# Optimization experiments

Hardware: AMD Instinct MI355X
Metric: run time of the kernel (lower is better)

## Reference

```python
import jax, jax.numpy as jnp
import numpy as np

# --- Config (Kimi/DeepSeek-style fine-grained MoE) ---
T = 4096        # num tokens
H = 1024        # hidden_size
I = 512         # moe_intermediate_size
E = 64          # num_experts
K = 8           # num_experts_per_token (top_k)
NG = 8          # num_expert_group
TKG = 4         # topk_group
NSH = 2         # num_shared_experts
IS = I * NSH    # shared-expert intermediate size
ROUTED_SCALE = 2.5


def setup_inputs() -> dict:
    key = jax.random.key(0)
    ks = jax.random.split(key, 7)
    s = 0.02
    return {
        "hidden_states": jax.random.normal(ks[0], (T, H), jnp.float32),
        "gate_w": jax.random.normal(ks[1], (E, H), jnp.float32) * s,          # router
        "e_bias": jax.random.normal(ks[2], (E,), jnp.float32) * 0.01,          # e_score_correction_bias
        "w1": jax.random.normal(ks[3], (E, H, 2 * I), jnp.float32) * s,       # per-expert gate_up
        "w2": jax.random.normal(ks[4], (E, I, H), jnp.float32) * s,           # per-expert down
        "sw_gu": jax.random.normal(ks[5], (H, 2 * IS), jnp.float32) * s,      # shared gate_up
        "sw_d": jax.random.normal(ks[6], (IS, H), jnp.float32) * s,           # shared down
    }


def _silu_and_mul(gu):
    d = gu.shape[-1] // 2
    return jax.nn.silu(gu[..., :d]) * gu[..., d:]


def _grouped_topk(scores, e_bias):
    """DeepSeek-V3/Kimi grouped top-k with sigmoid scoring + score-correction bias."""
    Tn = scores.shape[0]
    sfc = scores + e_bias[None, :]                       # scores_for_choice [T, E]
    # group score = sum of top-2 corrected scores inside each group
    grp = sfc.reshape(Tn, NG, E // NG)
    group_scores = jax.lax.top_k(grp, 2)[0].sum(-1)      # [T, NG]
    gidx = jax.lax.top_k(group_scores, TKG)[1]           # [T, TKG]
    gmask = jnp.zeros((Tn, NG), sfc.dtype).at[jnp.arange(Tn)[:, None], gidx].set(1.0)
    smask = jnp.repeat(gmask, E // NG, axis=1) > 0       # [T, E] bool
    tmp = jnp.where(smask, sfc, 0.0)                     # masked_fill(~mask, 0.0) as in vLLM
    topk_ids = jax.lax.top_k(tmp, K)[1]                  # [T, K]
    topk_w = jnp.take_along_axis(scores, topk_ids, axis=1)
    topk_w = topk_w / topk_w.sum(-1, keepdims=True)      # renormalize
    return topk_w, topk_ids


def _forward(x, gate_w, e_bias, w1, w2, sw_gu, sw_d):
    Tn, Hn = x.shape
    # shared experts (KimiMLP)
    shared = _silu_and_mul(x @ sw_gu) @ sw_d             # [T, H]
    # router
    logits = x @ gate_w.T                                # [T, E]
    scores = jax.nn.sigmoid(logits)
    topk_w, topk_ids = _grouped_topk(scores, e_bias)
    # dispatch: sort the T*K assignments by expert id -> grouped GEMM
    flat_ids = topk_ids.reshape(-1)                      # [T*K]
    order = jnp.argsort(flat_ids)                        # [T*K]
    tok = order // K                                     # token index of each sorted assignment
    xs = x[tok]                                          # [T*K, H] gathered tokens
    gsizes = jnp.bincount(flat_ids, length=E).astype(jnp.int32)
    gu = jax.lax.ragged_dot(xs, w1, gsizes)              # [T*K, 2I] grouped GEMM
    h = _silu_and_mul(gu)                                # [T*K, I]
    ys = jax.lax.ragged_dot(h, w2, gsizes)               # [T*K, H]
    # combine: scale by routing weight, scatter-add back to tokens
    flat_w = topk_w.reshape(-1)[order]                   # [T*K]
    routed = jnp.zeros((Tn, Hn), x.dtype).at[tok].add(ys * flat_w[:, None])
    return routed * ROUTED_SCALE + shared


def reference(hidden_states, gate_w, e_bias, w1, w2, sw_gu, sw_d):
    return _forward(hidden_states, gate_w, e_bias, w1, w2, sw_gu, sw_d)
```

## Files before the change

### kernel.cpp

```cpp
#include <hip/hip_runtime.h>
#include <cstdint>
#include <cstddef>

#define TT   4096
#define HH   1024
#define II   512
#define EE   64
#define KT   8
#define ISZ  1024
#define TKA  32768
#define MAXT 320

typedef __bf16 bf16x8 __attribute__((ext_vector_type(8)));
typedef float  f32x4  __attribute__((ext_vector_type(4)));

__device__ __forceinline__ unsigned short f2bf(float f) {
  unsigned u = __float_as_uint(f);
  u += 0x7fffu + ((u >> 16) & 1u);
  return (unsigned short)(u >> 16);
}

#define GLDS(gp, lp) __builtin_amdgcn_global_load_lds( \
    (const __attribute__((address_space(1))) void*)(gp), \
    (__attribute__((address_space(3))) void*)(lp), 16, 0, 0)

__global__ __launch_bounds__(256) void k_transpose(const float* __restrict__ in,
                                                   unsigned short* __restrict__ out,
                                                   int R, int C) {
  __shared__ float tile[64][65];
  long b = blockIdx.z;
  int r0 = blockIdx.x * 64, c0 = blockIdx.y * 64;
  const float* ip = in + b * (long)R * C;
  unsigned short* op = out + b * (long)R * C;
  int tc = threadIdx.x & 63, tr = threadIdx.x >> 6;
#pragma unroll
  for (int rr = 0; rr < 64; rr += 4)
    tile[tr + rr][tc] = ip[(long)(r0 + tr + rr) * C + (c0 + tc)];
  __syncthreads();
#pragma unroll
  for (int rr = 0; rr < 64; rr += 4)
    op[(long)(c0 + tr + rr) * R + (r0 + tc)] = f2bf(tile[tc][tr + rr]);
}

__global__ __launch_bounds__(256) void k_cvt(const float* __restrict__ in,
                                             unsigned short* __restrict__ out) {
  int i = blockIdx.x * 256 + threadIdx.x;
  float4 v = ((const float4*)in)[i];
  ushort4 o;
  o.x = f2bf(v.x); o.y = f2bf(v.y); o.z = f2bf(v.z); o.w = f2bf(v.w);
  ((ushort4*)out)[i] = o;
}

__global__ __launch_bounds__(256) void k_router(const float* __restrict__ x,
    const float* __restrict__ gw, const float* __restrict__ eb,
    int* __restrict__ topk_ids, float* __restrict__ topk_w, int* __restrict__ counts)
{
  __shared__ float xrow[HH];
  __shared__ float sc[EE];
  int t = blockIdx.x;
  int tid = threadIdx.x;
  for (int i = tid; i < HH; i += 256) xrow[i] = x[(long)t * HH + i];
  __syncthreads();
  int e = tid >> 2, q = tid & 3;
  const float* w = gw + (long)e * HH;
  double acc = 0.0, acc2 = 0.0;
  for (int i = q * 8; i < HH; i += 32) {
    float4 wa = *(const float4*)(w + i);
    float4 wb = *(const float4*)(w + i + 4);
    acc  += (double)wa.x * (double)xrow[i]
          + (double)wa.y * (double)xrow[i + 1]
          + (double)wa.z * (double)xrow[i + 2]
          + (double)wa.w * (double)xrow[i + 3];
    acc2 += (double)wb.x * (double)xrow[i + 4]
          + (double)wb.y * (double)xrow[i + 5]
          + (double)wb.z * (double)xrow[i + 6]
          + (double)wb.w * (double)xrow[i + 7];
  }
  acc += acc2;
  acc += __shfl_down(acc, 2);
  acc += __shfl_down(acc, 1);
  if (q == 0) sc[e] = (float)(1.0 / (1.0 + exp(-acc)));
  __syncthreads();
  if (tid < 64) {
    int lane = tid;
    float s = sc[lane];
    float sfc = s + eb[lane];
    float m1 = sfc, m2 = -1e30f;
#pragma unroll
    for (int d = 1; d < 8; d <<= 1) {
      float o1 = __shfl_xor(m1, d);
      float o2 = __shfl_xor(m2, d);
      float hi = fmaxf(m1, o1);
      float lo = fminf(m1, o1);
      m2 = fmaxf(lo, fmaxf(m2, o2));
      m1 = hi;
    }
    float gs = m1 + m2;
    int g = lane >> 3;
    int grank = 0;
#pragma unroll
    for (int j = 0; j < 8; j++) {
      float gj = __shfl(gs, j * 8);
      if (gj > gs || (gj == gs && j < g)) grank++;
    }
    bool gsel = grank < 4;
    float mv = gsel ? sfc : 0.0f;
    int rank = 0;
    for (int j = 0; j < 64; j++) {
      float vj = __shfl(mv, j);
      if (vj > mv || (vj == mv && j < lane)) rank++;
    }
    bool sel = rank < KT;
    float ssum = sel ? s : 0.0f;
#pragma unroll
    for (int d = 1; d < 64; d <<= 1) ssum += __shfl_xor(ssum, d);
    unsigned long long bal = __ballot(sel);
    if (sel) {
      int pos = __popcll(bal & ((1ull << lane) - 1ull));
      topk_ids[(long)t * KT + pos] = lane;
      topk_w[(long)t * KT + pos] = s / ssum;
      atomicAdd(&counts[lane], 1);
    }
  }
}

__global__ void k_offsets(const int* __restrict__ counts, int* __restrict__ offsets,
                          int* __restrict__ cursor, int* __restrict__ tile_e,
                          int* __restrict__ tile_r0)
{
  int lane = threadIdx.x;
  int c = counts[lane];
  int xs = c;
#pragma unroll
  for (int d = 1; d < 64; d <<= 1) { int y = __shfl_up(xs, d); if (lane >= d) xs += y; }
  int off = xs - c;
  offsets[lane] = off;
  cursor[lane] = off;
  if (lane == 63) offsets[EE] = xs;
  int nt = (c + 127) >> 7;
  int tp = nt;
#pragma unroll
  for (int d = 1; d < 64; d <<= 1) { int y = __shfl_up(tp, d); if (lane >= d) tp += y; }
  int tbase = tp - nt;
  for (int i = 0; i < nt; i++) { tile_e[tbase + i] = lane; tile_r0[tbase + i] = off + i * 128; }
  int total = __shfl(tp, 63);
  for (int i = total + lane; i < MAXT; i += 64) tile_e[i] = -1;
}

__global__ __launch_bounds__(256) void k_scatter(const int* __restrict__ ids,
    const float* __restrict__ tw, int* __restrict__ cursor,
    int* __restrict__ perm, float* __restrict__ wslot)
{
  int a = blockIdx.x * 256 + threadIdx.x;
  int e = ids[a];
  int pos = atomicAdd(&cursor[e], 1);
  perm[pos] = a >> 3;
  wslot[pos] = tw[a];
}

__global__ __launch_bounds__(256) void k_gemm_gu(
    const unsigned short* __restrict__ Abase, const int* __restrict__ perm,
    const unsigned short* __restrict__ Bbase, long eStride, int Kd, int upOff,
    unsigned short* __restrict__ Hout,
    const int* __restrict__ tile_e, const int* __restrict__ tile_r0,
    const int* __restrict__ eoff, int rowsTotal)
{
  __shared__ __align__(16) unsigned short lds[8192];
  int e = 0, row0, end;
  if (tile_e) {
    e = tile_e[blockIdx.x];
    if (e < 0) return;
    row0 = tile_r0[blockIdx.x];
    end = eoff[e + 1];
  } else { row0 = blockIdx.x * 128; end = rowsTotal; }
  const unsigned short* B = Bbase + (long)e * eStride;
  int n0 = blockIdx.y * 64;
  int tid = threadIdx.x, lane = tid & 63, wave = tid >> 6;
  int wm = wave >> 1, wn = wave & 1;
  int lr = lane >> 2, lk = (lane & 3) * 8;
  int r0a = row0 + wave * 32 + lr;
  int r1a = r0a + 16;
  int t0 = r0a < rowsTotal ? r0a : rowsTotal - 1;
  int t1 = r1a < rowsTotal ? r1a : rowsTotal - 1;
  if (perm) { t0 = perm[t0]; t1 = perm[t1]; }
  const unsigned short* ap0 = Abase + (long)t0 * Kd + lk;
  const unsigned short* ap1 = Abase + (long)t1 * Kd + lk;
  const unsigned short* bg = B + (long)(n0 + wave * 16 + lr) * Kd + lk;
  const unsigned short* bu = B + (long)(upOff + n0 + wave * 16 + lr) * Kd + lk;
  unsigned short* lA0 = lds + wave * 1024 + lane * 8;
  unsigned short* lBg = lds + 4096 + wave * 512 + lane * 8;
  unsigned short* lBu = lds + 6144 + wave * 512 + lane * 8;
  f32x4 acc[4][4];
  f32x4 z = {0.f, 0.f, 0.f, 0.f};
  for (int i = 0; i < 4; i++) for (int j = 0; j < 4; j++) acc[i][j] = z;
  int quad = lane >> 4, cl = lane & 15;
  for (int k0 = 0; k0 < Kd; k0 += 32) {
    __syncthreads();
    GLDS(ap0 + k0, lA0);
    GLDS(ap1 + k0, lA0 + 512);
    GLDS(bg + k0, lBg);
    GLDS(bu + k0, lBu);
    __syncthreads();
    bf16x8 af[4], bgf[2], buf2[2];
#pragma unroll
    for (int mi = 0; mi < 4; mi++)
      af[mi] = *(const bf16x8*)(lds + (wm * 64 + mi * 16 + cl) * 32 + quad * 8);
#pragma unroll
    for (int ni = 0; ni < 2; ni++) {
      bgf[ni]  = *(const bf16x8*)(lds + 4096 + (wn * 32 + ni * 16 + cl) * 32 + quad * 8);
      buf2[ni] = *(const bf16x8*)(lds + 6144 + (wn * 32 + ni * 16 + cl) * 32 + quad * 8);
    }
#pragma unroll
    for (int mi = 0; mi < 4; mi++) {
#pragma unroll
      for (int ni = 0; ni < 2; ni++) {
        acc[mi][ni]     = __builtin_amdgcn_mfma_f32_16x16x32_bf16(af[mi], bgf[ni],  acc[mi][ni],     0, 0, 0);
        acc[mi][ni + 2] = __builtin_amdgcn_mfma_f32_16x16x32_bf16(af[mi], buf2[ni], acc[mi][ni + 2], 0, 0, 0);
      }
    }
  }
#pragma unroll
  for (int mi = 0; mi < 4; mi++) {
#pragma unroll
    for (int j = 0; j < 2; j++) {
#pragma unroll
      for (int r = 0; r < 4; r++) {
        int row = row0 + wm * 64 + mi * 16 + quad * 4 + r;
        if (row < end) {
          float g = acc[mi][j][r], u = acc[mi][j + 2][r];
          float hv = g * (1.f / (1.f + __expf(-g))) * u;
          Hout[(long)row * upOff + (n0 + wn * 32 + j * 16 + cl)] = f2bf(hv);
        }
      }
    }
  }
}

__global__ __launch_bounds__(256) void k_gemm_down(
    const unsigned short* __restrict__ Abase,
    const unsigned short* __restrict__ Bbase, long eStride, int Kd,
    float* __restrict__ Out,
    const int* __restrict__ perm, const float* __restrict__ wslot,
    const int* __restrict__ tile_e, const int* __restrict__ tile_r0,
    const int* __restrict__ eoff, int rowsTotal, int doAtomic)
{
  __shared__ __align__(16) unsigned short lds[8192];
  int e = 0, row0, end;
  if (tile_e) {
    e = tile_e[blockIdx.x];
    if (e < 0) return;
    row0 = tile_r0[blockIdx.x];
    end = eoff[e + 1];
  } else { row0 = blockIdx.x * 128; end = rowsTotal; }
  const unsigned short* B = Bbase + (long)e * eStride;
  int n0 = blockIdx.y * 128;
  int tid = threadIdx.x, lane = tid & 63, wave = tid >> 6;
  int wm = wave >> 1, wn = wave & 1;
  int lr = lane >> 2, lk = (lane & 3) * 8;
  int r0a = row0 + wave * 32 + lr;
  int r1a = r0a + 16;
  int t0 = r0a < rowsTotal ? r0a : rowsTotal - 1;
  int t1 = r1a < rowsTotal ? r1a : rowsTotal - 1;
  const unsigned short* ap0 = Abase + (long)t0 * Kd + lk;
  const unsigned short* ap1 = Abase + (long)t1 * Kd + lk;
  const unsigned short* bp0 = B + (long)(n0 + wave * 32 + lr) * Kd + lk;
  const unsigned short* bp1 = bp0 + (long)16 * Kd;
  unsigned short* lA0 = lds + wave * 1024 + lane * 8;
  unsigned short* lB0 = lds + 4096 + wave * 1024 + lane * 8;
  f32x4 acc[4][4];
  f32x4 z = {0.f, 0.f, 0.f, 0.f};
  for (int i = 0; i < 4; i++) for (int j = 0; j < 4; j++) acc[i][j] = z;
  int quad = lane >> 4, cl = lane & 15;
  for (int k0 = 0; k0 < Kd; k0 += 32) {
    __syncthreads();
    GLDS(ap0 + k0, lA0);
    GLDS(ap1 + k0, lA0 + 512);
    GLDS(bp0 + k0, lB0);
    GLDS(bp1 + k0, lB0 + 512);
    __syncthreads();
    bf16x8 af[4], bfr[4];
#pragma unroll
    for (int mi = 0; mi < 4; mi++)
      af[mi] = *(const bf16x8*)(lds + (wm * 64 + mi * 16 + cl) * 32 + quad * 8);
#pragma unroll
    for (int ni = 0; ni < 4; ni++)
      bfr[ni] = *(const bf16x8*)(lds + 4096 + (wn * 64 + ni * 16 + cl) * 32 + quad * 8);
#pragma unroll
    for (int mi = 0; mi < 4; mi++)
#pragma unroll
      for (int ni = 0; ni < 4; ni++)
        acc[mi][ni] = __builtin_amdgcn_mfma_f32_16x16x32_bf16(af[mi], bfr[ni], acc[mi][ni], 0, 0, 0);
  }
#pragma unroll
  for (int mi = 0; mi < 4; mi++) {
    int rowb = row0 + wm * 64 + mi * 16 + quad * 4;
#pragma unroll
    for (int r = 0; r < 4; r++) {
      int row = rowb + r;
      if (row >= end) continue;
      long orow = row;
      float scale = 1.f;
      if (doAtomic) { orow = perm[row]; scale = wslot[row] * 2.5f; }
#pragma unroll
      for (int ni = 0; ni < 4; ni++) {
        int col = n0 + wn * 64 + ni * 16 + cl;
        float v = acc[mi][ni][r] * scale;
        if (doAtomic) unsafeAtomicAdd(&Out[orow * HH + col], v);
        else          Out[orow * HH + col] = v;
      }
    }
  }
}

extern "C" void kernel_launch(void* const* d_in, const int* in_sizes, int n_in,
                              void* d_out, int out_size, void* d_ws, size_t ws_size,
                              hipStream_t stream)
{
  const float* x   = (const float*)d_in[0];
  const float* gw  = (const float*)d_in[1];
  const float* eb  = (const float*)d_in[2];
  const float* w1  = (const float*)d_in[3];
  const float* w2  = (const float*)d_in[4];
  const float* sgu = (const float*)d_in[5];
  const float* sd  = (const float*)d_in[6];
  float* out = (float*)d_out;
  char* ws = (char*)d_ws;
  size_t off = 0;
  auto alloc = [&](size_t b) { void* p = ws + off; off += (b + 255) & ~(size_t)255; return p; };
  unsigned short* w1t  = (unsigned short*)alloc((size_t)EE * 2 * II * HH * 2);
  unsigned short* w2t  = (unsigned short*)alloc((size_t)EE * HH * II * 2);
  unsigned short* sgut = (unsigned short*)alloc((size_t)2 * ISZ * HH * 2);
  unsigned short* sdt  = (unsigned short*)alloc((size_t)HH * ISZ * 2);
  unsigned short* xb   = (unsigned short*)alloc((size_t)TT * HH * 2);
  unsigned short* hsb  = (unsigned short*)alloc((size_t)TT * ISZ * 2);
  unsigned short* hb   = (unsigned short*)alloc((size_t)TKA * II * 2);
  int*   tids   = (int*)alloc((size_t)TKA * 4);
  float* tw     = (float*)alloc((size_t)TKA * 4);
  int*   counts = (int*)alloc(256);
  int*   offs   = (int*)alloc(512);
  int*   cursor = (int*)alloc(256);
  int*   tile_e = (int*)alloc(MAXT * 4);
  int*   tile_r = (int*)alloc(MAXT * 4);
  int*   perm   = (int*)alloc((size_t)TKA * 4);
  float* wslot  = (float*)alloc((size_t)TKA * 4);

  hipMemsetAsync(counts, 0, 256, stream);
  dim3 b256(256);
  k_transpose<<<dim3(HH / 64, (2 * II) / 64, EE), b256, 0, stream>>>(w1, w1t, HH, 2 * II);
  k_transpose<<<dim3(II / 64, HH / 64, EE), b256, 0, stream>>>(w2, w2t, II, HH);
  k_transpose<<<dim3(HH / 64, (2 * ISZ) / 64, 1), b256, 0, stream>>>(sgu, sgut, HH, 2 * ISZ);
  k_transpose<<<dim3(ISZ / 64, HH / 64, 1), b256, 0, stream>>>(sd, sdt, ISZ, HH);
  k_cvt<<<dim3((TT * HH) / 1024), b256, 0, stream>>>(x, xb);
  k_router<<<dim3(TT), b256, 0, stream>>>(x, gw, eb, tids, tw, counts);
  k_offsets<<<dim3(1), dim3(64), 0, stream>>>(counts, offs, cursor, tile_e, tile_r);
  k_scatter<<<dim3(TKA / 256), b256, 0, stream>>>(tids, tw, cursor, perm, wslot);
  k_gemm_gu<<<dim3(MAXT, II / 64), b256, 0, stream>>>(xb, perm, w1t, (long)2 * II * HH, HH, II,
                                                      hb, tile_e, tile_r, offs, TKA);
  k_gemm_gu<<<dim3(TT / 128, ISZ / 64), b256, 0, stream>>>(xb, nullptr, sgut, 0, HH, ISZ,
                                                           hsb, nullptr, nullptr, nullptr, TT);
  k_gemm_down<<<dim3(TT / 128, HH / 128), b256, 0, stream>>>(hsb, sdt, 0, ISZ, out,
                                                             nullptr, nullptr, nullptr, nullptr,
                                                             nullptr, TT, 0);
  k_gemm_down<<<dim3(MAXT, HH / 128), b256, 0, stream>>>(hb, w2t, (long)HH * II, II, out,
                                                         perm, wslot, tile_e, tile_r, offs, TKA, 1);
}
```

Before: 1.003 ms.

## Replace atomic scatter-add with bf16 staging plus gather combine; swizzle LDS

The routed down-projection now writes weighted bf16 outputs per sorted slot into a staging buffer instead of doing float atomics into the output. A new combine kernel uses an inverse permutation to gather each token's K expert rows and add them to the shared-expert result. Separately, both GEMMs permute the k-chunk placement when filling LDS and read back with a matching swizzle to reduce bank conflicts. This removes atomic contention at the cost of an extra 64MB bf16 round trip and a bf16 rounding of the routed contributions before summation.

```diff
diff --git a/kernel.cpp b/kernel.cpp
--- a/kernel.cpp
+++ b/kernel.cpp
@@ -13,6 +13,7 @@
 
 typedef __bf16 bf16x8 __attribute__((ext_vector_type(8)));
 typedef float  f32x4  __attribute__((ext_vector_type(4)));
+typedef unsigned short us8v __attribute__((ext_vector_type(8)));
 
 __device__ __forceinline__ unsigned short f2bf(float f) {
   unsigned u = __float_as_uint(f);
@@ -23,6 +24,7 @@
 #define GLDS(gp, lp) __builtin_amdgcn_global_load_lds( \
     (const __attribute__((address_space(1))) void*)(gp), \
     (__attribute__((address_space(3))) void*)(lp), 16, 0, 0)
+
 
 __global__ __launch_bounds__(256) void k_transpose(const float* __restrict__ in,
                                                    unsigned short* __restrict__ out,
@@ -149,13 +151,14 @@
 
 __global__ __launch_bounds__(256) void k_scatter(const int* __restrict__ ids,
     const float* __restrict__ tw, int* __restrict__ cursor,
-    int* __restrict__ perm, float* __restrict__ wslot)
+    int* __restrict__ perm, float* __restrict__ wslot, int* __restrict__ inv)
 {
   int a = blockIdx.x * 256 + threadIdx.x;
   int e = ids[a];
   int pos = atomicAdd(&cursor[e], 1);
   perm[pos] = a >> 3;
   wslot[pos] = tw[a];
+  inv[a] = pos;
 }
 
 __global__ __launch_bounds__(256) void k_gemm_gu(
@@ -177,16 +180,17 @@
   int n0 = blockIdx.y * 64;
   int tid = threadIdx.x, lane = tid & 63, wave = tid >> 6;
   int wm = wave >> 1, wn = wave & 1;
-  int lr = lane >> 2, lk = (lane & 3) * 8;
+  int lr = lane >> 2;
+  int lkq = ((((lane & 3) - ((lane >> 3) & 3)) & 3)) * 8;
   int r0a = row0 + wave * 32 + lr;
   int r1a = r0a + 16;
   int t0 = r0a < rowsTotal ? r0a : rowsTotal - 1;
   int t1 = r1a < rowsTotal ? r1a : rowsTotal - 1;
   if (perm) { t0 = perm[t0]; t1 = perm[t1]; }
-  const unsigned short* ap0 = Abase + (long)t0 * Kd + lk;
-  const unsigned short* ap1 = Abase + (long)t1 * Kd + lk;
-  const unsigned short* bg = B + (long)(n0 + wave * 16 + lr) * Kd + lk;
-  const unsigned short* bu = B + (long)(upOff + n0 + wave * 16 + lr) * Kd + lk;
+  const unsigned short* ap0 = Abase + (long)t0 * Kd + lkq;
+  const unsigned short* ap1 = Abase + (long)t1 * Kd + lkq;
+  const unsigned short* bg = B + (long)(n0 + wave * 16 + lr) * Kd + lkq;
+  const unsigned short* bu = B + (long)(upOff + n0 + wave * 16 + lr) * Kd + lkq;
   unsigned short* lA0 = lds + wave * 1024 + lane * 8;
   unsigned short* lBg = lds + 4096 + wave * 512 + lane * 8;
   unsigned short* lBu = lds + 6144 + wave * 512 + lane * 8;
@@ -194,6 +198,7 @@
   f32x4 z = {0.f, 0.f, 0.f, 0.f};
   for (int i = 0; i < 4; i++) for (int j = 0; j < 4; j++) acc[i][j] = z;
   int quad = lane >> 4, cl = lane & 15;
+  int sw8 = ((quad + ((cl >> 1) & 3)) & 3) * 8;
   for (int k0 = 0; k0 < Kd; k0 += 32) {
     __syncthreads();
     GLDS(ap0 + k0, lA0);
@@ -204,11 +209,11 @@
     bf16x8 af[4], bgf[2], buf2[2];
 #pragma unroll
     for (int mi = 0; mi < 4; mi++)
-      af[mi] = *(const bf16x8*)(lds + (wm * 64 + mi * 16 + cl) * 32 + quad * 8);
+      af[mi] = *(const bf16x8*)(lds + (wm * 64 + mi * 16 + cl) * 32 + sw8);
 #pragma unroll
     for (int ni = 0; ni < 2; ni++) {
-      bgf[ni]  = *(const bf16x8*)(lds + 4096 + (wn * 32 + ni * 16 + cl) * 32 + quad * 8);
-      buf2[ni] = *(const bf16x8*)(lds + 6144 + (wn * 32 + ni * 16 + cl) * 32 + quad * 8);
+      bgf[ni]  = *(const bf16x8*)(lds + 4096 + (wn * 32 + ni * 16 + cl) * 32 + sw8);
+      buf2[ni] = *(const bf16x8*)(lds + 6144 + (wn * 32 + ni * 16 + cl) * 32 + sw8);
     }
 #pragma unroll
     for (int mi = 0; mi < 4; mi++) {
@@ -239,10 +244,9 @@
 __global__ __launch_bounds__(256) void k_gemm_down(
     const unsigned short* __restrict__ Abase,
     const unsigned short* __restrict__ Bbase, long eStride, int Kd,
-    float* __restrict__ Out,
-    const int* __restrict__ perm, const float* __restrict__ wslot,
+    void* __restrict__ Outv, const float* __restrict__ wslot,
     const int* __restrict__ tile_e, const int* __restrict__ tile_r0,
-    const int* __restrict__ eoff, int rowsTotal, int doAtomic)
+    const int* __restrict__ eoff, int rowsTotal, int mode)
 {
   __shared__ __align__(16) unsigned short lds[8192];
   int e = 0, row0, end;
@@ -256,14 +260,15 @@
   int n0 = blockIdx.y * 128;
   int tid = threadIdx.x, lane = tid & 63, wave = tid >> 6;
   int wm = wave >> 1, wn = wave & 1;
-  int lr = lane >> 2, lk = (lane & 3) * 8;
+  int lr = lane >> 2;
+  int lkq = ((((lane & 3) - ((lane >> 3) & 3)) & 3)) * 8;
   int r0a = row0 + wave * 32 + lr;
   int r1a = r0a + 16;
   int t0 = r0a < rowsTotal ? r0a : rowsTotal - 1;
   int t1 = r1a < rowsTotal ? r1a : rowsTotal - 1;
-  const unsigned short* ap0 = Abase + (long)t0 * Kd + lk;
-  const unsigned short* ap1 = Abase + (long)t1 * Kd + lk;
-  const unsigned short* bp0 = B + (long)(n0 + wave * 32 + lr) * Kd + lk;
+  const unsigned short* ap0 = Abase + (long)t0 * Kd + lkq;
+  const unsigned short* ap1 = Abase + (long)t1 * Kd + lkq;
+  const unsigned short* bp0 = B + (long)(n0 + wave * 32 + lr) * Kd + lkq;
   const unsigned short* bp1 = bp0 + (long)16 * Kd;
   unsigned short* lA0 = lds + wave * 1024 + lane * 8;
   unsigned short* lB0 = lds + 4096 + wave * 1024 + lane * 8;
@@ -271,6 +276,7 @@
   f32x4 z = {0.f, 0.f, 0.f, 0.f};
   for (int i = 0; i < 4; i++) for (int j = 0; j < 4; j++) acc[i][j] = z;
   int quad = lane >> 4, cl = lane & 15;
+  int sw8 = ((quad + ((cl >> 1) & 3)) & 3) * 8;
   for (int k0 = 0; k0 < Kd; k0 += 32) {
     __syncthreads();
     GLDS(ap0 + k0, lA0);
@@ -281,10 +287,10 @@
     bf16x8 af[4], bfr[4];
 #pragma unroll
     for (int mi = 0; mi < 4; mi++)
-      af[mi] = *(const bf16x8*)(lds + (wm * 64 + mi * 16 + cl) * 32 + quad * 8);
+      af[mi] = *(const bf16x8*)(lds + (wm * 64 + mi * 16 + cl) * 32 + sw8);
 #pragma unroll
     for (int ni = 0; ni < 4; ni++)
-      bfr[ni] = *(const bf16x8*)(lds + 4096 + (wn * 64 + ni * 16 + cl) * 32 + quad * 8);
+      bfr[ni] = *(const bf16x8*)(lds + 4096 + (wn * 64 + ni * 16 + cl) * 32 + sw8);
 #pragma unroll
     for (int mi = 0; mi < 4; mi++)
 #pragma unroll
@@ -298,18 +304,44 @@
     for (int r = 0; r < 4; r++) {
       int row = rowb + r;
       if (row >= end) continue;
-      long orow = row;
-      float scale = 1.f;
-      if (doAtomic) { orow = perm[row]; scale = wslot[row] * 2.5f; }
-#pragma unroll
-      for (int ni = 0; ni < 4; ni++) {
-        int col = n0 + wn * 64 + ni * 16 + cl;
-        float v = acc[mi][ni][r] * scale;
-        if (doAtomic) unsafeAtomicAdd(&Out[orow * HH + col], v);
-        else          Out[orow * HH + col] = v;
+      if (mode) {
+        unsigned short* Y = (unsigned short*)Outv;
+        float scale = wslot[row] * 2.5f;
+#pragma unroll
+        for (int ni = 0; ni < 4; ni++) {
+          int col = n0 + wn * 64 + ni * 16 + cl;
+          Y[(long)row * HH + col] = f2bf(acc[mi][ni][r] * scale);
+        }
+      } else {
+        float* O = (float*)Outv;
+#pragma unroll
+        for (int ni = 0; ni < 4; ni++) {
+          int col = n0 + wn * 64 + ni * 16 + cl;
+          O[(long)row * HH + col] = acc[mi][ni][r];
+        }
       }
     }
   }
+}
+
+__global__ __launch_bounds__(256) void k_combine(const unsigned short* __restrict__ ys,
+    const int* __restrict__ inv, float* __restrict__ out)
+{
+  int idx = blockIdx.x * 256 + threadIdx.x;
+  int t = idx >> 7, c0 = (idx & 127) << 3;
+  const int* ip = inv + (long)t * KT;
+  float* op = out + (long)t * HH + c0;
+  float4 o0 = *(float4*)op;
+  float4 o1 = *(float4*)(op + 4);
+  float a[8] = {o0.x, o0.y, o0.z, o0.w, o1.x, o1.y, o1.z, o1.w};
+#pragma unroll
+  for (int k = 0; k < KT; k++) {
+    us8v v = *(const us8v*)(ys + (long)ip[k] * HH + c0);
+#pragma unroll
+    for (int j = 0; j < 8; j++) a[j] += __uint_as_float((unsigned)v[j] << 16);
+  }
+  *(float4*)op = make_float4(a[0], a[1], a[2], a[3]);
+  *(float4*)(op + 4) = make_float4(a[4], a[5], a[6], a[7]);
 }
 
 extern "C" void kernel_launch(void* const* d_in, const int* in_sizes, int n_in,
@@ -334,6 +366,7 @@
   unsigned short* xb   = (unsigned short*)alloc((size_t)TT * HH * 2);
   unsigned short* hsb  = (unsigned short*)alloc((size_t)TT * ISZ * 2);
   unsigned short* hb   = (unsigned short*)alloc((size_t)TKA * II * 2);
+  unsigned short* ys   = (unsigned short*)alloc((size_t)TKA * HH * 2);
   int*   tids   = (int*)alloc((size_t)TKA * 4);
   float* tw     = (float*)alloc((size_t)TKA * 4);
   int*   counts = (int*)alloc(256);
@@ -343,6 +376,7 @@
   int*   tile_r = (int*)alloc(MAXT * 4);
   int*   perm   = (int*)alloc((size_t)TKA * 4);
   float* wslot  = (float*)alloc((size_t)TKA * 4);
+  int*   inv    = (int*)alloc((size_t)TKA * 4);
 
   hipMemsetAsync(counts, 0, 256, stream);
   dim3 b256(256);
@@ -353,14 +387,14 @@
   k_cvt<<<dim3((TT * HH) / 1024), b256, 0, stream>>>(x, xb);
   k_router<<<dim3(TT), b256, 0, stream>>>(x, gw, eb, tids, tw, counts);
   k_offsets<<<dim3(1), dim3(64), 0, stream>>>(counts, offs, cursor, tile_e, tile_r);
-  k_scatter<<<dim3(TKA / 256), b256, 0, stream>>>(tids, tw, cursor, perm, wslot);
+  k_scatter<<<dim3(TKA / 256), b256, 0, stream>>>(tids, tw, cursor, perm, wslot, inv);
   k_gemm_gu<<<dim3(MAXT, II / 64), b256, 0, stream>>>(xb, perm, w1t, (long)2 * II * HH, HH, II,
                                                       hb, tile_e, tile_r, offs, TKA);
+  k_gemm_down<<<dim3(MAXT, HH / 128), b256, 0, stream>>>(hb, w2t, (long)HH * II, II, (void*)ys,
+                                                         wslot, tile_e, tile_r, offs, TKA, 1);
   k_gemm_gu<<<dim3(TT / 128, ISZ / 64), b256, 0, stream>>>(xb, nullptr, sgut, 0, HH, ISZ,
                                                            hsb, nullptr, nullptr, nullptr, TT);
-  k_gemm_down<<<dim3(TT / 128, HH / 128), b256, 0, stream>>>(hsb, sdt, 0, ISZ, out,
-                                                             nullptr, nullptr, nullptr, nullptr,
-                                                             nullptr, TT, 0);
-  k_gemm_down<<<dim3(MAXT, HH / 128), b256, 0, stream>>>(hb, w2t, (long)HH * II, II, out,
-                                                         perm, wslot, tile_e, tile_r, offs, TKA, 1);
-}
+  k_gemm_down<<<dim3(TT / 128, HH / 128), b256, 0, stream>>>(hsb, sdt, 0, ISZ, (void*)out,
+                                                             nullptr, nullptr, nullptr, nullptr, TT, 0);
+  k_combine<<<dim3(TT * 128 / 256), b256, 0, stream>>>(ys, inv, out);
+}
```

After: 969.6 us. 3.4% less time.
